# Kernel optimization log

Measured on AMD Instinct MI355X. Metric: run time of the kernel, lower is better.

The kernel has to match this reference:

```python
import jax, jax.numpy as jnp
import numpy as np

NUM_EXPERTS = 64
TOP_K = 2
AUX_COEF = 0.001
Z_COEF = 0.001


def setup_inputs() -> dict:
    key = jax.random.key(0)
    k1, k2 = jax.random.split(key)
    hidden_states = jax.random.normal(k1, (16384, 4096), dtype=jnp.float32)
    W_gate = jax.random.normal(k2, (NUM_EXPERTS, 4096), dtype=jnp.float32) * 0.02
    return {"hidden_states": hidden_states, "W_gate": W_gate}


def reference(hidden_states, W_gate):
    # Gate GEMM: [N, H] x [E, H]^T -> [N, E]
    router_logits = jnp.einsum('nh,eh->ne', hidden_states, W_gate)
    router_probs = jax.nn.softmax(router_logits, axis=-1)

    # Top-k selection + renormalization
    expert_weights, expert_indices = jax.lax.top_k(router_probs, TOP_K)
    expert_weights = expert_weights / jnp.sum(expert_weights, axis=-1, keepdims=True)

    # Load-balancing loss: num_experts * sum_i f_i * P_i
    num_tokens = router_probs.shape[0]
    one_hot = jax.nn.one_hot(expert_indices, NUM_EXPERTS, dtype=jnp.float32)  # [N, K, E]
    tokens_per_expert = one_hot.sum(axis=(0, 1))  # [E]
    f = tokens_per_expert / (num_tokens * TOP_K)
    P = router_probs.mean(axis=0)
    lb_loss = NUM_EXPERTS * jnp.sum(f * P)

    # Z-loss: mean of logsumexp(logits)^2
    log_z = jax.nn.logsumexp(router_logits, axis=-1)
    z_loss = jnp.mean(log_z ** 2)

    aux_loss = AUX_COEF * lb_loss + Z_COEF * z_loss
    return expert_weights, expert_indices, aux_loss
```

## Files before the change

kernel.cpp:

```cpp
#include <hip/hip_runtime.h>
#include <hip/hip_bf16.h>

#define NTOK 16384
#define HD   4096
#define NE   64

#define TTILE 32
#define NBLK (NTOK / TTILE)
#define BK    64
#define NITP  (HD / BK)

#define NIT  (HD / 32)

#define SAB 40
#define SA2 72
#define SL  68

#define WS_ACC_FLOATS 192
#define B_ELEMS (NE * HD)

typedef __bf16 bf16x8 __attribute__((ext_vector_type(8)));
typedef __bf16 bf16x4 __attribute__((ext_vector_type(4)));
typedef float  f32x4  __attribute__((ext_vector_type(4)));

__device__ __forceinline__ f32x4 mfma16(bf16x8 a, bf16x8 b, f32x4 c) {
    return __builtin_amdgcn_mfma_f32_16x16x32_bf16(a, b, c, 0, 0, 0);
}

__device__ __forceinline__ void cvt_split(float4 v, bf16x4& hi, bf16x4& lo) {
    float x[4] = {v.x, v.y, v.z, v.w};
    #pragma unroll
    for (int e = 0; e < 4; ++e) {
        __bf16 h = (__bf16)x[e];
        hi[e] = h;
        lo[e] = (__bf16)(x[e] - (float)h);
    }
}

__device__ __forceinline__ void cvt8(float4 x0, float4 x1, bf16x8& hi, bf16x8& lo) {
    bf16x4 h, l;
    cvt_split(x0, h, l);
    #pragma unroll
    for (int e = 0; e < 4; ++e) { hi[e] = h[e]; lo[e] = l[e]; }
    cvt_split(x1, h, l);
    #pragma unroll
    for (int e = 0; e < 4; ++e) { hi[4 + e] = h[e]; lo[4 + e] = l[e]; }
}

__global__ void zero_ws_kernel(float* ws) {
    int i = threadIdx.x;
    if (i < 129) ws[i] = 0.0f;
}

__global__ __launch_bounds__(256) void prep_kernel(
    const float* __restrict__ Wg, float* __restrict__ ws)
{
    const int tid = threadIdx.x;
    if (blockIdx.x == 0 && tid < 129) ws[tid] = 0.0f;
    __bf16* Bhi = (__bf16*)(ws + WS_ACC_FLOATS);
    __bf16* Blo = Bhi + B_ELEMS;
    const int i = (blockIdx.x * 256 + tid) * 8;
    float4 v0 = *(const float4*)(Wg + i);
    float4 v1 = *(const float4*)(Wg + i + 4);
    bf16x4 h0, l0, h1, l1;
    cvt_split(v0, h0, l0);
    cvt_split(v1, h1, l1);
    *(bf16x4*)(Bhi + i)     = h0;
    *(bf16x4*)(Bhi + i + 4) = h1;
    *(bf16x4*)(Blo + i)     = l0;
    *(bf16x4*)(Blo + i + 4) = l1;
}

__global__ __launch_bounds__(256) void router_pre_kernel(
    const float* __restrict__ hs,
    const __bf16* __restrict__ Bhi,
    const __bf16* __restrict__ Blo,
    float* __restrict__ out,
    float* __restrict__ ws)
{
    __shared__ __bf16 sAhi[2][TTILE * SA2];
    __shared__ __bf16 sAlo[2][TTILE * SA2];
    __shared__ __bf16 sBhi[2][NE * SA2];
    __shared__ __bf16 sBlo[2][NE * SA2];
    __shared__ float  sLog[TTILE * SL];
    __shared__ float  sInv[TTILE];
    __shared__ float  sPp[4 * 64];
    __shared__ float  sCnt[64];
    __shared__ float  sZ;

    const int tid = threadIdx.x;
    const int t0  = blockIdx.x * TTILE;

    if (tid < 64) sCnt[tid] = 0.0f;
    if (tid == 0) sZ = 0.0f;

    const int rowA = tid >> 3;
    const int colA = (tid & 7) * 8;
    const float* gA = hs + (size_t)(t0 + rowA) * HD + colA;
    const int oAw = rowA * SA2 + colA;

    const int eb = tid >> 2;
    const int cB = (tid & 3) * 8;
    const __bf16* gBh = Bhi + (size_t)eb * HD + cB;
    const __bf16* gBl = Blo + (size_t)eb * HD + cB;
    const int oBw = eb * SA2 + cB;

    const int lane = tid & 63;
    const int wv   = tid >> 6;
    const int wr   = (wv >> 1) * 16;
    const int wc   = (wv & 1) * 32;
    const int fm   = lane & 15;
    const int fq   = lane >> 4;
    const int fk   = fq * 8;

    f32x4 acc[2];
    acc[0] = (f32x4){0.f, 0.f, 0.f, 0.f};
    acc[1] = (f32x4){0.f, 0.f, 0.f, 0.f};

    {
        float4 a0 = *(const float4*)(gA);
        float4 a1 = *(const float4*)(gA + 4);
        bf16x8 h, l;
        cvt8(a0, a1, h, l);
        *(bf16x8*)&sAhi[0][oAw] = h;
        *(bf16x8*)&sAlo[0][oAw] = l;
        *(bf16x8*)&sBhi[0][oBw]      = *(const bf16x8*)(gBh);
        *(bf16x8*)&sBhi[0][oBw + 32] = *(const bf16x8*)(gBh + 32);
        *(bf16x8*)&sBlo[0][oBw]      = *(const bf16x8*)(gBl);
        *(bf16x8*)&sBlo[0][oBw + 32] = *(const bf16x8*)(gBl + 32);
    }
    __syncthreads();

    #pragma unroll 2
    for (int it = 0; it < NITP; ++it) {
        const int cur = it & 1;
        const bool more = (it + 1) < NITP;

        float4 na0, na1;
        bf16x8 nb0, nb1, nb2, nb3;
        if (more) {
            const int k0 = (it + 1) * BK;
            na0 = *(const float4*)(gA + k0);
            na1 = *(const float4*)(gA + k0 + 4);
            nb0 = *(const bf16x8*)(gBh + k0);
            nb1 = *(const bf16x8*)(gBh + k0 + 32);
            nb2 = *(const bf16x8*)(gBl + k0);
            nb3 = *(const bf16x8*)(gBl + k0 + 32);
        }

        #pragma unroll
        for (int kk = 0; kk < 2; ++kk) {
            const int ao = (wr + fm) * SA2 + kk * 32 + fk;
            bf16x8 ahi = *(const bf16x8*)&sAhi[cur][ao];
            bf16x8 alo = *(const bf16x8*)&sAlo[cur][ao];
            const int bo0 = (wc + fm) * SA2 + kk * 32 + fk;
            const int bo1 = (wc + 16 + fm) * SA2 + kk * 32 + fk;
            bf16x8 bh0 = *(const bf16x8*)&sBhi[cur][bo0];
            bf16x8 bh1 = *(const bf16x8*)&sBhi[cur][bo1];
            bf16x8 bl0 = *(const bf16x8*)&sBlo[cur][bo0];
            bf16x8 bl1 = *(const bf16x8*)&sBlo[cur][bo1];
            acc[0] = mfma16(ahi, bh0, acc[0]);
            acc[1] = mfma16(ahi, bh1, acc[1]);
            acc[0] = mfma16(ahi, bl0, acc[0]);
            acc[1] = mfma16(ahi, bl1, acc[1]);
            acc[0] = mfma16(alo, bh0, acc[0]);
            acc[1] = mfma16(alo, bh1, acc[1]);
            acc[0] = mfma16(alo, bl0, acc[0]);
            acc[1] = mfma16(alo, bl1, acc[1]);
        }

        if (more) {
            const int nb = cur ^ 1;
            bf16x8 h, l;
            cvt8(na0, na1, h, l);
            *(bf16x8*)&sAhi[nb][oAw] = h;
            *(bf16x8*)&sAlo[nb][oAw] = l;
            *(bf16x8*)&sBhi[nb][oBw]      = nb0;
            *(bf16x8*)&sBhi[nb][oBw + 32] = nb1;
            *(bf16x8*)&sBlo[nb][oBw]      = nb2;
            *(bf16x8*)&sBlo[nb][oBw + 32] = nb3;
        }
        __syncthreads();
    }

    #pragma unroll
    for (int j = 0; j < 2; ++j)
        #pragma unroll
        for (int r = 0; r < 4; ++r) {
            const int tokl = wr + fq * 4 + r;
            const int expl = wc + j * 16 + fm;
            sLog[tokl * SL + expl] = acc[j][r];
        }
    __syncthreads();

    const int g = tid >> 3;
    const int l = tid & 7;
    float* Lrow = &sLog[g * SL + l * 8];
    float lv[8];
    float m = -3.0e38f;
    #pragma unroll
    for (int c = 0; c < 8; ++c) { lv[c] = Lrow[c]; m = fmaxf(m, lv[c]); }
    m = fmaxf(m, __shfl_xor(m, 1, 64));
    m = fmaxf(m, __shfl_xor(m, 2, 64));
    m = fmaxf(m, __shfl_xor(m, 4, 64));

    float v1 = -3.0e38f, v2 = -3.0e38f; int i1 = 0, i2 = 0;
    float ssum = 0.0f;
    #pragma unroll
    for (int c = 0; c < 8; ++c) {
        const float val = lv[c]; const int idx = l * 8 + c;
        const float ev = __expf(val - m);
        Lrow[c] = ev;
        ssum += ev;
        if (val > v1) { v2 = v1; i2 = i1; v1 = val; i1 = idx; }
        else if (val > v2) { v2 = val; i2 = idx; }
    }
    ssum += __shfl_xor(ssum, 1, 64);
    ssum += __shfl_xor(ssum, 2, 64);
    ssum += __shfl_xor(ssum, 4, 64);

    #pragma unroll
    for (int s = 1; s <= 4; s <<= 1) {
        const float ov1 = __shfl_xor(v1, s, 64);
        const int   oi1 = __shfl_xor(i1, s, 64);
        const float ov2 = __shfl_xor(v2, s, 64);
        const int   oi2 = __shfl_xor(i2, s, 64);
        float n1, n2; int ni1, ni2;
        const bool ofirst = (ov1 > v1) || (ov1 == v1 && oi1 < i1);
        if (ofirst) {
            n1 = ov1; ni1 = oi1;
            const bool osec = (ov2 > v1) || (ov2 == v1 && oi2 < i1);
            n2 = osec ? ov2 : v1; ni2 = osec ? oi2 : i1;
        } else {
            n1 = v1; ni1 = i1;
            const bool asec = (v2 > ov1) || (v2 == ov1 && i2 < oi1);
            n2 = asec ? v2 : ov1; ni2 = asec ? i2 : oi1;
        }
        v1 = n1; i1 = ni1; v2 = n2; i2 = ni2;
    }

    if (l == 0) {
        const float e1 = __expf(v1 - m), e2 = __expf(v2 - m);
        const float winv = 1.0f / (e1 + e2);
        const int token = t0 + g;
        out[2 * token]     = e1 * winv;
        out[2 * token + 1] = e2 * winv;
        out[2 * NTOK + 2 * token]     = (float)i1;
        out[2 * NTOK + 2 * token + 1] = (float)i2;
        const float lse = m + __logf(ssum);
        atomicAdd(&sZ, lse * lse);
        atomicAdd(&sCnt[i1], 1.0f);
        atomicAdd(&sCnt[i2], 1.0f);
        sInv[g] = 1.0f / ssum;
    }
    __syncthreads();

    {
        const int e = tid & 63;
        const int q = tid >> 6;
        float part = 0.0f;
        #pragma unroll
        for (int t = 0; t < 8; ++t) {
            const int tok = q * 8 + t;
            part += sLog[tok * SL + e] * sInv[tok];
        }
        sPp[q * 64 + e] = part;
    }
    __syncthreads();
    if (tid < 64) {
        const float ps = sPp[tid] + sPp[64 + tid] + sPp[128 + tid] + sPp[192 + tid];
        atomicAdd(&ws[tid], ps);
        atomicAdd(&ws[64 + tid], sCnt[tid]);
    }
    if (tid == 0) atomicAdd(&ws[128], sZ);
}

__global__ __launch_bounds__(256) void router_fb_kernel(
    const float* __restrict__ hs,
    const float* __restrict__ Wg,
    float* __restrict__ out,
    float* __restrict__ ws)
{
    __shared__ __bf16 sAhi[2][TTILE * SAB];
    __shared__ __bf16 sAlo[2][TTILE * SAB];
    __shared__ __bf16 sBhi[2][NE * SAB];
    __shared__ __bf16 sBlo[2][NE * SAB];
    __shared__ float  sLog[TTILE * SL];
    __shared__ float  sInv[TTILE];
    __shared__ float  sPp[4 * 64];
    __shared__ float  sCnt[64];
    __shared__ float  sZ;

    const int tid = threadIdx.x;
    const int t0  = blockIdx.x * TTILE;

    if (tid < 64) sCnt[tid] = 0.0f;
    if (tid == 0) sZ = 0.0f;

    const int r1 = tid >> 3;
    const int c4 = (tid & 7) * 4;
    const float* gA = hs + (size_t)(t0 + r1) * HD + c4;
    const float* gB = Wg + (size_t)r1 * HD + c4;
    const int oA  = r1 * SAB + c4;
    const int oB1 = r1 * SAB + c4;
    const int oB2 = (r1 + 32) * SAB + c4;

    const int lane = tid & 63;
    const int wv   = tid >> 6;
    const int wr   = (wv >> 1) * 16;
    const int wc   = (wv & 1) * 32;
    const int fm   = lane & 15;
    const int fq   = lane >> 4;
    const int fk   = fq * 8;

    f32x4 acc[2];
    acc[0] = (f32x4){0.f, 0.f, 0.f, 0.f};
    acc[1] = (f32x4){0.f, 0.f, 0.f, 0.f};

    {
        float4 a0 = *(const float4*)(gA);
        float4 b0 = *(const float4*)(gB);
        float4 b1 = *(const float4*)(gB + 32 * HD);
        bf16x4 h, l;
        cvt_split(a0, h, l); *(bf16x4*)&sAhi[0][oA]  = h; *(bf16x4*)&sAlo[0][oA]  = l;
        cvt_split(b0, h, l); *(bf16x4*)&sBhi[0][oB1] = h; *(bf16x4*)&sBlo[0][oB1] = l;
        cvt_split(b1, h, l); *(bf16x4*)&sBhi[0][oB2] = h; *(bf16x4*)&sBlo[0][oB2] = l;
    }
    __syncthreads();

    for (int it = 0; it < NIT; ++it) {
        const int cur = it & 1;
        const bool more = (it + 1) < NIT;
        float4 na0, nb0, nb1;
        if (more) {
            const int k0 = (it + 1) * 32;
            na0 = *(const float4*)(gA + k0);
            nb0 = *(const float4*)(gB + k0);
            nb1 = *(const float4*)(gB + 32 * HD + k0);
        }

        bf16x8 ahi, alo, bhi[2], blo[2];
        {
            const int aoff = (wr + fm) * SAB + fk;
            ahi = *(const bf16x8*)&sAhi[cur][aoff];
            alo = *(const bf16x8*)&sAlo[cur][aoff];
        }
        #pragma unroll
        for (int j = 0; j < 2; ++j) {
            const int boff = (wc + j * 16 + fm) * SAB + fk;
            bhi[j] = *(const bf16x8*)&sBhi[cur][boff];
            blo[j] = *(const bf16x8*)&sBlo[cur][boff];
        }
        #pragma unroll
        for (int j = 0; j < 2; ++j) {
            acc[j] = mfma16(ahi, bhi[j], acc[j]);
            acc[j] = mfma16(ahi, blo[j], acc[j]);
            acc[j] = mfma16(alo, bhi[j], acc[j]);
            acc[j] = mfma16(alo, blo[j], acc[j]);
        }

        if (more) {
            const int nb = cur ^ 1;
            bf16x4 h, l;
            cvt_split(na0, h, l); *(bf16x4*)&sAhi[nb][oA]  = h; *(bf16x4*)&sAlo[nb][oA]  = l;
            cvt_split(nb0, h, l); *(bf16x4*)&sBhi[nb][oB1] = h; *(bf16x4*)&sBlo[nb][oB1] = l;
            cvt_split(nb1, h, l); *(bf16x4*)&sBhi[nb][oB2] = h; *(bf16x4*)&sBlo[nb][oB2] = l;
        }
        __syncthreads();
    }

    #pragma unroll
    for (int j = 0; j < 2; ++j)
        #pragma unroll
        for (int r = 0; r < 4; ++r) {
            const int tokl = wr + fq * 4 + r;
            const int expl = wc + j * 16 + fm;
            sLog[tokl * SL + expl] = acc[j][r];
        }
    __syncthreads();

    const int g = tid >> 3;
    const int l = tid & 7;
    float* Lrow = &sLog[g * SL + l * 8];
    float lv[8];
    float m = -3.0e38f;
    #pragma unroll
    for (int c = 0; c < 8; ++c) { lv[c] = Lrow[c]; m = fmaxf(m, lv[c]); }
    m = fmaxf(m, __shfl_xor(m, 1, 64));
    m = fmaxf(m, __shfl_xor(m, 2, 64));
    m = fmaxf(m, __shfl_xor(m, 4, 64));

    float v1 = -3.0e38f, v2 = -3.0e38f; int i1 = 0, i2 = 0;
    float ssum = 0.0f;
    #pragma unroll
    for (int c = 0; c < 8; ++c) {
        const float val = lv[c]; const int idx = l * 8 + c;
        const float ev = __expf(val - m);
        Lrow[c] = ev;
        ssum += ev;
        if (val > v1) { v2 = v1; i2 = i1; v1 = val; i1 = idx; }
        else if (val > v2) { v2 = val; i2 = idx; }
    }
    ssum += __shfl_xor(ssum, 1, 64);
    ssum += __shfl_xor(ssum, 2, 64);
    ssum += __shfl_xor(ssum, 4, 64);

    #pragma unroll
    for (int s = 1; s <= 4; s <<= 1) {
        const float ov1 = __shfl_xor(v1, s, 64);
        const int   oi1 = __shfl_xor(i1, s, 64);
        const float ov2 = __shfl_xor(v2, s, 64);
        const int   oi2 = __shfl_xor(i2, s, 64);
        float n1, n2; int ni1, ni2;
        const bool ofirst = (ov1 > v1) || (ov1 == v1 && oi1 < i1);
        if (ofirst) {
            n1 = ov1; ni1 = oi1;
            const bool osec = (ov2 > v1) || (ov2 == v1 && oi2 < i1);
            n2 = osec ? ov2 : v1; ni2 = osec ? oi2 : i1;
        } else {
            n1 = v1; ni1 = i1;
            const bool asec = (v2 > ov1) || (v2 == ov1 && i2 < oi1);
            n2 = asec ? v2 : ov1; ni2 = asec ? i2 : oi1;
        }
        v1 = n1; i1 = ni1; v2 = n2; i2 = ni2;
    }

    if (l == 0) {
        const float e1 = __expf(v1 - m), e2 = __expf(v2 - m);
        const float winv = 1.0f / (e1 + e2);
        const int token = t0 + g;
        out[2 * token]     = e1 * winv;
        out[2 * token + 1] = e2 * winv;
        out[2 * NTOK + 2 * token]     = (float)i1;
        out[2 * NTOK + 2 * token + 1] = (float)i2;
        const float lse = m + __logf(ssum);
        atomicAdd(&sZ, lse * lse);
        atomicAdd(&sCnt[i1], 1.0f);
        atomicAdd(&sCnt[i2], 1.0f);
        sInv[g] = 1.0f / ssum;
    }
    __syncthreads();

    {
        const int e = tid & 63;
        const int q = tid >> 6;
        float part = 0.0f;
        #pragma unroll
        for (int t = 0; t < 8; ++t) {
            const int tok = q * 8 + t;
            part += sLog[tok * SL + e] * sInv[tok];
        }
        sPp[q * 64 + e] = part;
    }
    __syncthreads();
    if (tid < 64) {
        const float ps = sPp[tid] + sPp[64 + tid] + sPp[128 + tid] + sPp[192 + tid];
        atomicAdd(&ws[tid], ps);
        atomicAdd(&ws[64 + tid], sCnt[tid]);
    }
    if (tid == 0) atomicAdd(&ws[128], sZ);
}

__global__ void finalize_kernel(const float* __restrict__ ws, float* __restrict__ out) {
    const int e = threadIdx.x;
    const float P = ws[e] * (1.0f / NTOK);
    const float f = ws[64 + e] * (1.0f / (NTOK * 2));
    float term = f * P;
    #pragma unroll
    for (int s = 32; s >= 1; s >>= 1) term += __shfl_xor(term, s, 64);
    if (e == 0) {
        const float lb = 64.0f * term;
        const float z  = ws[128] * (1.0f / NTOK);
        out[4 * NTOK] = 0.001f * lb + 0.001f * z;
    }
}

extern "C" void kernel_launch(void* const* d_in, const int* in_sizes, int n_in,
                              void* d_out, int out_size, void* d_ws, size_t ws_size,
                              hipStream_t stream) {
    const float* hs = (const float*)d_in[0];
    const float* Wg = (const float*)d_in[1];
    float* out = (float*)d_out;
    float* ws  = (float*)d_ws;

    const size_t need = (size_t)WS_ACC_FLOATS * sizeof(float)
                      + (size_t)B_ELEMS * 2 * sizeof(__bf16);
    if (ws_size >= need) {
        const __bf16* Bhi = (const __bf16*)(ws + WS_ACC_FLOATS);
        const __bf16* Blo = Bhi + B_ELEMS;
        hipLaunchKernelGGL(prep_kernel, dim3(128), dim3(256), 0, stream, Wg, ws);
        hipLaunchKernelGGL(router_pre_kernel, dim3(NBLK), dim3(256), 0, stream,
                           hs, Bhi, Blo, out, ws);
    } else {
        hipLaunchKernelGGL(zero_ws_kernel, dim3(1), dim3(256), 0, stream, ws);
        hipLaunchKernelGGL(router_fb_kernel, dim3(NBLK), dim3(256), 0, stream,
                           hs, Wg, out, ws);
    }
    hipLaunchKernelGGL(finalize_kernel, dim3(1), dim3(64), 0, stream, ws, out);
}
```

Baseline: 394.1 us.

## Deepen global prefetch to two tiles with explicit barriers in gate GEMM

Restructures the K loop of the router GEMM so two register sets hold global loads issued two iterations ahead, alternating between the two shared-memory buffers. It replaces __syncthreads with an explicit lgkmcnt wait plus s_barrier, and adds sched_barrier fences so the compiler cannot move the loads past the MFMA block. It also adds a min-2-blocks-per-SM launch bound. The aim is to hide global memory latency in a bandwidth-bound kernel, at the cost of more registers and possible spills under the occupancy bound.

Measured after the change: 379.5 us. 3.7% less time.

```diff
diff --git a/kernel.cpp b/kernel.cpp
--- a/kernel.cpp
+++ b/kernel.cpp
@@ -71,7 +71,7 @@
     *(bf16x4*)(Blo + i + 4) = l1;
 }
 
-__global__ __launch_bounds__(256) void router_pre_kernel(
+__global__ __launch_bounds__(256, 2) void router_pre_kernel(
     const float* __restrict__ hs,
     const __bf16* __restrict__ Bhi,
     const __bf16* __restrict__ Blo,
@@ -117,71 +117,88 @@
     acc[0] = (f32x4){0.f, 0.f, 0.f, 0.f};
     acc[1] = (f32x4){0.f, 0.f, 0.f, 0.f};
 
-    {
-        float4 a0 = *(const float4*)(gA);
-        float4 a1 = *(const float4*)(gA + 4);
-        bf16x8 h, l;
-        cvt8(a0, a1, h, l);
-        *(bf16x8*)&sAhi[0][oAw] = h;
-        *(bf16x8*)&sAlo[0][oAw] = l;
-        *(bf16x8*)&sBhi[0][oBw]      = *(const bf16x8*)(gBh);
-        *(bf16x8*)&sBhi[0][oBw + 32] = *(const bf16x8*)(gBh + 32);
-        *(bf16x8*)&sBlo[0][oBw]      = *(const bf16x8*)(gBl);
-        *(bf16x8*)&sBlo[0][oBw + 32] = *(const bf16x8*)(gBl + 32);
-    }
-    __syncthreads();
-
-    #pragma unroll 2
-    for (int it = 0; it < NITP; ++it) {
-        const int cur = it & 1;
-        const bool more = (it + 1) < NITP;
-
-        float4 na0, na1;
-        bf16x8 nb0, nb1, nb2, nb3;
-        if (more) {
-            const int k0 = (it + 1) * BK;
-            na0 = *(const float4*)(gA + k0);
-            na1 = *(const float4*)(gA + k0 + 4);
-            nb0 = *(const bf16x8*)(gBh + k0);
-            nb1 = *(const bf16x8*)(gBh + k0 + 32);
-            nb2 = *(const bf16x8*)(gBl + k0);
-            nb3 = *(const bf16x8*)(gBl + k0 + 32);
-        }
-
-        #pragma unroll
-        for (int kk = 0; kk < 2; ++kk) {
-            const int ao = (wr + fm) * SA2 + kk * 32 + fk;
-            bf16x8 ahi = *(const bf16x8*)&sAhi[cur][ao];
-            bf16x8 alo = *(const bf16x8*)&sAlo[cur][ao];
-            const int bo0 = (wc + fm) * SA2 + kk * 32 + fk;
-            const int bo1 = (wc + 16 + fm) * SA2 + kk * 32 + fk;
-            bf16x8 bh0 = *(const bf16x8*)&sBhi[cur][bo0];
-            bf16x8 bh1 = *(const bf16x8*)&sBhi[cur][bo1];
-            bf16x8 bl0 = *(const bf16x8*)&sBlo[cur][bo0];
-            bf16x8 bl1 = *(const bf16x8*)&sBlo[cur][bo1];
-            acc[0] = mfma16(ahi, bh0, acc[0]);
-            acc[1] = mfma16(ahi, bh1, acc[1]);
-            acc[0] = mfma16(ahi, bl0, acc[0]);
-            acc[1] = mfma16(ahi, bl1, acc[1]);
-            acc[0] = mfma16(alo, bh0, acc[0]);
-            acc[1] = mfma16(alo, bh1, acc[1]);
-            acc[0] = mfma16(alo, bl0, acc[0]);
-            acc[1] = mfma16(alo, bl1, acc[1]);
-        }
-
-        if (more) {
-            const int nb = cur ^ 1;
-            bf16x8 h, l;
-            cvt8(na0, na1, h, l);
-            *(bf16x8*)&sAhi[nb][oAw] = h;
-            *(bf16x8*)&sAlo[nb][oAw] = l;
-            *(bf16x8*)&sBhi[nb][oBw]      = nb0;
-            *(bf16x8*)&sBhi[nb][oBw + 32] = nb1;
-            *(bf16x8*)&sBlo[nb][oBw]      = nb2;
-            *(bf16x8*)&sBlo[nb][oBw + 32] = nb3;
-        }
-        __syncthreads();
-    }
+    float4 R0a0, R0a1; bf16x8 R0b0, R0b1, R0b2, R0b3;
+    float4 R1a0, R1a1; bf16x8 R1b0, R1b1, R1b2, R1b3;
+
+#define LOADT(R, t)                                                      \
+    {                                                                    \
+        const int k0 = (t) * BK;                                         \
+        R##a0 = *(const float4*)(gA + k0);                               \
+        R##a1 = *(const float4*)(gA + k0 + 4);                           \
+        R##b0 = *(const bf16x8*)(gBh + k0);                              \
+        R##b1 = *(const bf16x8*)(gBh + k0 + 32);                         \
+        R##b2 = *(const bf16x8*)(gBl + k0);                              \
+        R##b3 = *(const bf16x8*)(gBl + k0 + 32);                         \
+    }
+
+#define WRITET(R, buf)                                                   \
+    {                                                                    \
+        bf16x8 h_, l_;                                                   \
+        cvt8(R##a0, R##a1, h_, l_);                                      \
+        *(bf16x8*)&sAhi[buf][oAw] = h_;                                  \
+        *(bf16x8*)&sAlo[buf][oAw] = l_;                                  \
+        *(bf16x8*)&sBhi[buf][oBw]      = R##b0;                          \
+        *(bf16x8*)&sBhi[buf][oBw + 32] = R##b1;                          \
+        *(bf16x8*)&sBlo[buf][oBw]      = R##b2;                          \
+        *(bf16x8*)&sBlo[buf][oBw + 32] = R##b3;                          \
+    }
+
+#define COMPUTE(buf)                                                     \
+    {                                                                    \
+        _Pragma("unroll")                                                \
+        for (int kk = 0; kk < 2; ++kk) {                                 \
+            const int ao = (wr + fm) * SA2 + kk * 32 + fk;               \
+            bf16x8 ahi = *(const bf16x8*)&sAhi[buf][ao];                 \
+            bf16x8 alo = *(const bf16x8*)&sAlo[buf][ao];                 \
+            const int bo0 = (wc + fm) * SA2 + kk * 32 + fk;              \
+            const int bo1 = (wc + 16 + fm) * SA2 + kk * 32 + fk;         \
+            bf16x8 bh0 = *(const bf16x8*)&sBhi[buf][bo0];                \
+            bf16x8 bh1 = *(const bf16x8*)&sBhi[buf][bo1];                \
+            bf16x8 bl0 = *(const bf16x8*)&sBlo[buf][bo0];                \
+            bf16x8 bl1 = *(const bf16x8*)&sBlo[buf][bo1];                \
+            acc[0] = mfma16(ahi, bh0, acc[0]);                           \
+            acc[1] = mfma16(ahi, bh1, acc[1]);                           \
+            acc[0] = mfma16(ahi, bl0, acc[0]);                           \
+            acc[1] = mfma16(ahi, bl1, acc[1]);                           \
+            acc[0] = mfma16(alo, bh0, acc[0]);                           \
+            acc[1] = mfma16(alo, bh1, acc[1]);                           \
+            acc[0] = mfma16(alo, bl0, acc[0]);                           \
+            acc[1] = mfma16(alo, bl1, acc[1]);                           \
+        }                                                                \
+    }
+
+#define BAR()                                                            \
+    {                                                                    \
+        asm volatile("s_waitcnt lgkmcnt(0)" ::: "memory");               \
+        __builtin_amdgcn_s_barrier();                                    \
+        __builtin_amdgcn_sched_barrier(0);                               \
+    }
+
+    LOADT(R0, 0)
+    LOADT(R1, 1)
+    WRITET(R0, 0)
+    BAR()
+
+    for (int it = 0; it < NITP; it += 2) {
+        const bool m2 = (it + 2) < NITP;
+        const bool m3 = (it + 3) < NITP;
+
+        if (m2) LOADT(R0, it + 2)
+        __builtin_amdgcn_sched_barrier(0);
+        COMPUTE(0)
+        WRITET(R1, 1)
+        BAR()
+
+        if (m3) LOADT(R1, it + 3)
+        __builtin_amdgcn_sched_barrier(0);
+        COMPUTE(1)
+        if (m2) WRITET(R0, 0)
+        BAR()
+    }
+#undef LOADT
+#undef WRITET
+#undef COMPUTE
+#undef BAR
 
     #pragma unroll
     for (int j = 0; j < 2; ++j)
```
